# Optimization experiments

Measured on AMD Instinct MI355X. Metric: run time of the kernel, lower is better.

Reference implementation:

```python
import jax, jax.numpy as jnp
import numpy as np

B, S, H = 16, 1024, 64
HEADS, DH = 4, 16
EPS = 1e-5


def _layernorm(x, g, b):
    mu = jnp.mean(x, axis=-1, keepdims=True)
    var = jnp.mean(jnp.square(x - mu), axis=-1, keepdims=True)
    return (x - mu) * jax.lax.rsqrt(var + EPS) * g + b


def setup_inputs() -> dict:
    key = jax.random.key(0)
    ks = jax.random.split(key, 16)
    s = 1.0 / np.sqrt(H)
    inp = {
        'x': jax.random.normal(ks[0], (B, S, H), dtype=jnp.float32),
        'lengths': jax.random.randint(ks[1], (B,), 1, S + 1, dtype=jnp.int32),
        'atten': jnp.zeros((1,), dtype=jnp.float32),  # unused placeholder arg
        'Wq': jax.random.normal(ks[2], (H, H), dtype=jnp.float32) * s,
        'bq': jnp.zeros((H,), dtype=jnp.float32),
        'Wk': jax.random.normal(ks[3], (H, H), dtype=jnp.float32) * s,
        'bk': jnp.zeros((H,), dtype=jnp.float32),
        'Wv': jax.random.normal(ks[4], (H, H), dtype=jnp.float32) * s,
        'bv': jnp.zeros((H,), dtype=jnp.float32),
        'W1': jax.random.normal(ks[5], (H, H), dtype=jnp.float32) * s,
        'b1': jnp.zeros((H,), dtype=jnp.float32),
        'W2': jax.random.normal(ks[6], (H, H), dtype=jnp.float32) * s,
        'b2': jnp.zeros((H,), dtype=jnp.float32),
        'g1': jnp.ones((H,), dtype=jnp.float32),
        'be1': jnp.zeros((H,), dtype=jnp.float32),
        'g2': jnp.ones((H,), dtype=jnp.float32),
        'be2': jnp.zeros((H,), dtype=jnp.float32),
    }
    return inp


def reference(x, lengths, atten, Wq, bq, Wk, bk, Wv, bv, W1, b1, W2, b2, g1, be1, g2, be2):
    del atten  # overwritten in original forward before any use
    b, s, h = x.shape

    def proj(W, bias):
        p = x @ W.T + bias  # [b,s,h]
        return p.reshape(b, s, HEADS, DH).transpose(0, 2, 1, 3)  # [b,nh,s,dh]

    q, k, v = proj(Wq, bq), proj(Wk, bk), proj(Wv, bv)
    scores = jnp.einsum('bhqd,bhkd->bhqk', q, k) / np.float32(np.sqrt(h))

    causal = jnp.tril(jnp.ones((s, s), dtype=bool))  # [s,s]
    pos = jnp.arange(s)
    valid = pos[None, :] < lengths[:, None]  # [b,s]
    mask = causal[None, None] & valid[:, None, None, :] & valid[:, None, :, None]

    logits = jnp.where(mask, scores, jnp.float32(-1e30))
    att = jax.nn.softmax(logits, axis=-1) * mask  # zero fully-masked rows (NaN->0 trick)

    out = jnp.einsum('bhqk,bhkd->bhqd', att, v)
    out = out.transpose(0, 2, 1, 3).reshape(b, s, h)

    out_1 = x + out  # dropout is identity in eval mode
    out_1_norm = _layernorm(out_1, g1, be1)
    ff = jax.nn.gelu(out_1_norm @ W1.T + b1, approximate=False) @ W2.T + b2
    y_prim = _layernorm(out_1_norm + ff, g2, be2)

    atten_mean = jnp.mean(att, axis=1)  # [b,s,s], detached in original
    return (y_prim, atten_mean)
```

## Files before the change

### kernel.cpp

```cpp
#include <hip/hip_runtime.h>

#define NB 16
#define NS 1024
#define NHID 64
#define NHEADS 4
#define NDH 16
#define LN_EPS 1e-5f
#define QSCALE 0.18033688011112f

using v2h  = __attribute__((ext_vector_type(2))) _Float16;
using v4h  = __attribute__((ext_vector_type(4))) _Float16;
using v4f  = __attribute__((ext_vector_type(4))) float;

__device__ __forceinline__ v4h cvt4h(float4 a) {
    v4h r; r[0] = (_Float16)a.x; r[1] = (_Float16)a.y;
    r[2] = (_Float16)a.z; r[3] = (_Float16)a.w; return r;
}

__global__ __launch_bounds__(256) void qkv_mfma_kernel(
    const float* __restrict__ x,
    const float* __restrict__ Wq, const float* __restrict__ bq,
    const float* __restrict__ Wk, const float* __restrict__ bk,
    const float* __restrict__ Wv, const float* __restrict__ bv,
    _Float16* __restrict__ qh, _Float16* __restrict__ kh,
    _Float16* __restrict__ vt)
{
    const int t = threadIdx.x;
    const int w = t >> 6, l = t & 63;
    const int n16 = l & 15, g = l >> 4;
    const int rt = (int)blockIdx.x * 4 + w;
    const int srow0 = rt * 16;
    const int b = srow0 >> 10, s0 = srow0 & 1023;
    const size_t sg = (size_t)srow0 + n16;

    v4h xa[4];
    #pragma unroll
    for (int kb = 0; kb < 4; ++kb)
        xa[kb] = cvt4h(*(const float4*)&x[sg * 64 + kb * 16 + 4 * g]);

    #pragma unroll
    for (int m = 0; m < 3; ++m) {
        const float* W  = (m == 0) ? Wq : (m == 1) ? Wk : Wv;
        const float* bb = (m == 0) ? bq : (m == 1) ? bk : bv;
        #pragma unroll
        for (int mb = 0; mb < 4; ++mb) {
            const float4 bv4 = *(const float4*)&bb[mb * 16 + 4 * g];
            v4f acc = {bv4.x, bv4.y, bv4.z, bv4.w};
            #pragma unroll
            for (int kb = 0; kb < 4; ++kb) {
                v4h wf = cvt4h(*(const float4*)&W[(size_t)(mb * 16 + n16) * 64 + kb * 16 + 4 * g]);
                acc = __builtin_amdgcn_mfma_f32_16x16x16f16(wf, xa[kb], acc, 0, 0, 0);
            }
            const size_t hb = (size_t)(b * NHEADS + mb);
            if (m == 0) {
                v4h r = {(_Float16)(acc[0] * QSCALE), (_Float16)(acc[1] * QSCALE),
                         (_Float16)(acc[2] * QSCALE), (_Float16)(acc[3] * QSCALE)};
                *(v4h*)&qh[(hb * NS + s0 + n16) * NDH + 4 * g] = r;
            } else if (m == 1) {
                v4h r = {(_Float16)acc[0], (_Float16)acc[1], (_Float16)acc[2], (_Float16)acc[3]};
                *(v4h*)&kh[(hb * NS + s0 + n16) * NDH + 4 * g] = r;
            } else {
                #pragma unroll
                for (int i = 0; i < 4; ++i)
                    vt[(hb * NDH + 4 * g + i) * NS + s0 + n16] = (_Float16)acc[i];
            }
        }
    }
}

__global__ __launch_bounds__(1024, 8) void attn_ffn_kernel(
    const _Float16* __restrict__ qh, const _Float16* __restrict__ kh,
    const _Float16* __restrict__ vt, const int* __restrict__ lengths,
    const float* __restrict__ x,
    const float* __restrict__ W1, const float* __restrict__ b1,
    const float* __restrict__ W2, const float* __restrict__ b2,
    const float* __restrict__ g1, const float* __restrict__ be1,
    const float* __restrict__ g2, const float* __restrict__ be2,
    float* __restrict__ amean,
    float* __restrict__ y)
{
    __shared__ __align__(16) _Float16 Plds[2][NHEADS][16][72];
    __shared__ float zlds[4][NHEADS][16];
    __shared__ float aout_s[16][68];
    __shared__ __align__(16) _Float16 h1s[4][16][20];
    __shared__ float ln2s[4][16][2];

    const int t = threadIdx.x;
    const int wv = t >> 6;
    const int h  = wv & 3;
    const int kq = wv >> 2;
    const int l  = t & 63;
    const int g = l >> 4, n16 = l & 15;
    const int qt = 63 - (int)blockIdx.x;
    const int b  = blockIdx.y;
    const int len = lengths[b];
    const int q0 = qt << 4;
    const int qA_ = q0 + n16;
    const bool qvA = qA_ < len;
    const bool lenFA = len >= q0 + 16;

    const size_t hbase = ((size_t)(b * NHEADS + h)) * NS;
    const v4h QA = *(const v4h*)&qh[(hbase + qA_) * NDH + 4 * g];

    const int nkA = (len <= q0) ? 0 : min(q0 + 16, len);
    const int ntA = (nkA + 63) >> 6;
    const v4f z4v = {0.f, 0.f, 0.f, 0.f};

    float ZA = 0.f;
    for (int tile = 0; tile < ntA; ++tile) {
        const int ks = (tile << 6) + (kq << 4);
        if (ks >= nkA) continue;
        const v4h K = *(const v4h*)&kh[(hbase + ks + n16) * NDH + 4 * g];
        v4f st = __builtin_amdgcn_mfma_f32_16x16x16f16(K, QA, z4v, 0, 0, 0);
        if (lenFA && (ks + 15 <= q0)) {
            ZA += exp2f(st[0]) + exp2f(st[1]) + exp2f(st[2]) + exp2f(st[3]);
        } else {
            #pragma unroll
            for (int i = 0; i < 4; ++i) {
                int kg = ks + 4 * g + i;
                ZA += (qvA && kg <= qA_) ? exp2f(st[i]) : 0.f;
            }
        }
    }
    ZA += __shfl_xor(ZA, 16, 64); ZA += __shfl_xor(ZA, 32, 64);
    if (l < 16) zlds[kq][h][n16] = ZA;
    __syncthreads();
    const float ztA = zlds[0][h][n16] + zlds[1][h][n16]
                    + zlds[2][h][n16] + zlds[3][h][n16];
    const float izA = (ztA > 0.f) ? 1.f / ztA : 0.f;

    v4f oA = z4v;
    const int pc = (kq << 4) + 4 * g;
    for (int tile = 0; tile < ntA; ++tile) {
        const int k0 = tile << 6;
        const int ks = k0 + (kq << 4);
        const int par = tile & 1;
        v4h phA = {(_Float16)0.f, (_Float16)0.f, (_Float16)0.f, (_Float16)0.f};
        if (ks < nkA) {
            const v4h K = *(const v4h*)&kh[(hbase + ks + n16) * NDH + 4 * g];
            const v4h V = *(const v4h*)&vt[(((size_t)(b * NHEADS + h)) * NDH + n16) * NS + ks + 4 * g];
            v4f st = __builtin_amdgcn_mfma_f32_16x16x16f16(K, QA, z4v, 0, 0, 0);
            float p0, p1, p2, p3;
            if (lenFA && (ks + 15 <= q0)) {
                p0 = exp2f(st[0]) * izA; p1 = exp2f(st[1]) * izA;
                p2 = exp2f(st[2]) * izA; p3 = exp2f(st[3]) * izA;
            } else {
                const int kg = ks + 4 * g;
                p0 = (qvA && kg + 0 <= qA_) ? exp2f(st[0]) * izA : 0.f;
                p1 = (qvA && kg + 1 <= qA_) ? exp2f(st[1]) * izA : 0.f;
                p2 = (qvA && kg + 2 <= qA_) ? exp2f(st[2]) * izA : 0.f;
                p3 = (qvA && kg + 3 <= qA_) ? exp2f(st[3]) * izA : 0.f;
            }
            phA[0] = (_Float16)p0; phA[1] = (_Float16)p1;
            phA[2] = (_Float16)p2; phA[3] = (_Float16)p3;
            oA = __builtin_amdgcn_mfma_f32_16x16x16f16(phA, V, oA, 0, 0, 0);
        }
        *(v4h*)&Plds[par][h][n16][pc] = phA;
        __syncthreads();
        {
            const int r = t >> 6, c = t & 63;
            float s = (float)Plds[par][0][r][c] + (float)Plds[par][1][r][c]
                    + (float)Plds[par][2][r][c] + (float)Plds[par][3][r][c];
            amean[((size_t)(b * NS + q0 + r)) * NS + k0 + c] = 0.25f * s;
        }
    }
    __syncthreads();

    float* obuf = (float*)Plds;
    {
        float* p = &obuf[(wv * 64 + l) * 4];
        p[0] = oA[0]; p[1] = oA[1]; p[2] = oA[2]; p[3] = oA[3];
    }
    __syncthreads();
    if (kq == 0) {
        #pragma unroll
        for (int kq2 = 1; kq2 < 4; ++kq2) {
            const float* p = &obuf[(((h + 4 * kq2) * 64) + l) * 4];
            oA[0] += p[0]; oA[1] += p[1]; oA[2] += p[2]; oA[3] += p[3];
        }
        #pragma unroll
        for (int i = 0; i < 4; ++i)
            aout_s[4 * g + i][h * 16 + n16] = oA[i];
    }
    __syncthreads();

    const bool fact = wv < 4;
    const int fw = wv;
    const size_t row = (size_t)(b * NS + q0) + n16;

    v4h n1h[4];
    float4 n1self;
    if (fact) {
        float4 o1f[4];
        #pragma unroll
        for (int kb = 0; kb < 4; ++kb) {
            float4 xv = *(const float4*)&x[row * 64 + kb * 16 + 4 * g];
            float4 av = *(const float4*)&aout_s[n16][kb * 16 + 4 * g];
            o1f[kb] = make_float4(xv.x + av.x, xv.y + av.y, xv.z + av.z, xv.w + av.w);
        }
        float s = 0.f;
        #pragma unroll
        for (int kb = 0; kb < 4; ++kb) s += o1f[kb].x + o1f[kb].y + o1f[kb].z + o1f[kb].w;
        s += __shfl_xor(s, 16, 64); s += __shfl_xor(s, 32, 64);
        const float mu = s * (1.f / 64.f);
        float vs = 0.f;
        #pragma unroll
        for (int kb = 0; kb < 4; ++kb) {
            float a = o1f[kb].x - mu, bb = o1f[kb].y - mu, c = o1f[kb].z - mu, d = o1f[kb].w - mu;
            vs += a * a + bb * bb + c * c + d * d;
        }
        vs += __shfl_xor(vs, 16, 64); vs += __shfl_xor(vs, 32, 64);
        const float rs = rsqrtf(vs * (1.f / 64.f) + LN_EPS);
        #pragma unroll
        for (int kb = 0; kb < 4; ++kb) {
            float4 gv  = *(const float4*)&g1[kb * 16 + 4 * g];
            float4 bev = *(const float4*)&be1[kb * 16 + 4 * g];
            float4 nv;
            nv.x = (o1f[kb].x - mu) * rs * gv.x + bev.x;
            nv.y = (o1f[kb].y - mu) * rs * gv.y + bev.y;
            nv.z = (o1f[kb].z - mu) * rs * gv.z + bev.z;
            nv.w = (o1f[kb].w - mu) * rs * gv.w + bev.w;
            n1h[kb] = cvt4h(nv);
            if (kb == fw) n1self = nv;
        }
        const float4 b1v = *(const float4*)&b1[fw * 16 + 4 * g];
        v4f acc = {b1v.x, b1v.y, b1v.z, b1v.w};
        #pragma unroll
        for (int kb = 0; kb < 4; ++kb) {
            v4h wf = cvt4h(*(const float4*)&W1[(size_t)(fw * 16 + n16) * 64 + kb * 16 + 4 * g]);
            acc = __builtin_amdgcn_mfma_f32_16x16x16f16(wf, n1h[kb], acc, 0, 0, 0);
        }
        v4h hh;
        #pragma unroll
        for (int i = 0; i < 4; ++i) {
            float a = acc[i];
            hh[i] = (_Float16)(0.5f * a * (1.f + erff(a * 0.70710678118654752f)));
        }
        *(v4h*)&h1s[fw][n16][4 * g] = hh;
    } else {
        const int kz = ntA << 6;
        const int nz4 = (NS - kz) >> 2;
        const float4 zf = make_float4(0.f, 0.f, 0.f, 0.f);
        const int tt = (wv - 4) * 64 + l;
        for (int r = 0; r < 16; ++r)
            for (int c4 = tt; c4 < nz4; c4 += 768)
                *(float4*)&amean[((size_t)(b * NS + q0 + r)) * NS + kz + c4 * 4] = zf;
    }
    __syncthreads();

    float4 zrow;
    if (fact) {
        const float4 b2v = *(const float4*)&b2[fw * 16 + 4 * g];
        v4f acc = {b2v.x, b2v.y, b2v.z, b2v.w};
        #pragma unroll
        for (int db = 0; db < 4; ++db) {
            v4h hf = *(const v4h*)&h1s[db][n16][4 * g];
            v4h wf = cvt4h(*(const float4*)&W2[(size_t)(fw * 16 + n16) * 64 + db * 16 + 4 * g]);
            acc = __builtin_amdgcn_mfma_f32_16x16x16f16(wf, hf, acc, 0, 0, 0);
        }
        zrow = make_float4(n1self.x + acc[0], n1self.y + acc[1],
                           n1self.z + acc[2], n1self.w + acc[3]);
        float s2 = zrow.x + zrow.y + zrow.z + zrow.w;
        float q2 = zrow.x * zrow.x + zrow.y * zrow.y + zrow.z * zrow.z + zrow.w * zrow.w;
        s2 += __shfl_xor(s2, 16, 64); s2 += __shfl_xor(s2, 32, 64);
        q2 += __shfl_xor(q2, 16, 64); q2 += __shfl_xor(q2, 32, 64);
        if (g == 0) { ln2s[fw][n16][0] = s2; ln2s[fw][n16][1] = q2; }
    }
    __syncthreads();
    if (fact) {
        const float ts = ln2s[0][n16][0] + ln2s[1][n16][0]
                       + ln2s[2][n16][0] + ln2s[3][n16][0];
        const float tq = ln2s[0][n16][1] + ln2s[1][n16][1]
                       + ln2s[2][n16][1] + ln2s[3][n16][1];
        const float mu2 = ts * (1.f / 64.f);
        const float var2 = tq * (1.f / 64.f) - mu2 * mu2;
        const float rs2 = rsqrtf(var2 + LN_EPS);
        float4 gv  = *(const float4*)&g2[fw * 16 + 4 * g];
        float4 bev = *(const float4*)&be2[fw * 16 + 4 * g];
        float4 yv;
        yv.x = (zrow.x - mu2) * rs2 * gv.x + bev.x;
        yv.y = (zrow.y - mu2) * rs2 * gv.y + bev.y;
        yv.z = (zrow.z - mu2) * rs2 * gv.z + bev.z;
        yv.w = (zrow.w - mu2) * rs2 * gv.w + bev.w;
        *(float4*)&y[row * 64 + fw * 16 + 4 * g] = yv;
    }
}

extern "C" void kernel_launch(void* const* d_in, const int* in_sizes, int n_in,
                              void* d_out, int out_size, void* d_ws, size_t ws_size,
                              hipStream_t stream) {
    const float* x   = (const float*)d_in[0];
    const int* lengths = (const int*)d_in[1];
    const float* Wq  = (const float*)d_in[3];
    const float* bq  = (const float*)d_in[4];
    const float* Wk  = (const float*)d_in[5];
    const float* bk  = (const float*)d_in[6];
    const float* Wv  = (const float*)d_in[7];
    const float* bv  = (const float*)d_in[8];
    const float* W1  = (const float*)d_in[9];
    const float* b1  = (const float*)d_in[10];
    const float* W2  = (const float*)d_in[11];
    const float* b2  = (const float*)d_in[12];
    const float* g1  = (const float*)d_in[13];
    const float* be1 = (const float*)d_in[14];
    const float* g2  = (const float*)d_in[15];
    const float* be2 = (const float*)d_in[16];

    float* y     = (float*)d_out;
    float* amean = y + (size_t)NB * NS * NHID;

    const size_t nqkv = (size_t)NB * NHEADS * NS * NDH;
    _Float16* qhw = (_Float16*)d_ws;
    _Float16* khw = qhw + nqkv;
    _Float16* vtw = khw + nqkv;

    hipLaunchKernelGGL(qkv_mfma_kernel, dim3(NB * NS / 64), dim3(256), 0, stream,
                       x, Wq, bq, Wk, bk, Wv, bv, qhw, khw, vtw);
    hipLaunchKernelGGL(attn_ffn_kernel, dim3(64, NB), dim3(1024), 0, stream,
                       qhw, khw, vtw, lengths, x,
                       W1, b1, W2, b2, g1, be1, g2, be2,
                       amean, y);
}
```

Before: 60.90 us.

## Give each wave all four heads per key chunk and drop per-tile barriers

The attention block now uses 8 waves instead of 16. Each wave handles every head for a strided set of 16-key chunks, so the head-mean of attention probabilities is summed in registers and written directly to global memory. This removes the per-tile LDS staging and __syncthreads round-trips that previously combined heads. The cost is more registers per thread (four Q fragments and four accumulators), a two-stage LDS reduction of partial outputs, and fewer threads per block for zero-filling the unused part of amean.

```diff
diff --git a/kernel.cpp b/kernel.cpp
--- a/kernel.cpp
+++ b/kernel.cpp
@@ -8,7 +8,6 @@
 #define LN_EPS 1e-5f
 #define QSCALE 0.18033688011112f
 
-using v2h  = __attribute__((ext_vector_type(2))) _Float16;
 using v4h  = __attribute__((ext_vector_type(4))) _Float16;
 using v4f  = __attribute__((ext_vector_type(4))) float;
 
@@ -68,7 +67,7 @@
     }
 }
 
-__global__ __launch_bounds__(1024, 8) void attn_ffn_kernel(
+__global__ __launch_bounds__(512, 8) void attn_ffn_kernel(
     const _Float16* __restrict__ qh, const _Float16* __restrict__ kh,
     const _Float16* __restrict__ vt, const int* __restrict__ lengths,
     const float* __restrict__ x,
@@ -79,16 +78,14 @@
     float* __restrict__ amean,
     float* __restrict__ y)
 {
-    __shared__ __align__(16) _Float16 Plds[2][NHEADS][16][72];
-    __shared__ float zlds[4][NHEADS][16];
+    __shared__ __align__(16) float obuf[4][4][64][4];
+    __shared__ float zlds[8][4][16];
     __shared__ float aout_s[16][68];
     __shared__ __align__(16) _Float16 h1s[4][16][20];
     __shared__ float ln2s[4][16][2];
 
     const int t = threadIdx.x;
-    const int wv = t >> 6;
-    const int h  = wv & 3;
-    const int kq = wv >> 2;
+    const int w8 = t >> 6;
     const int l  = t & 63;
     const int g = l >> 4, n16 = l & 15;
     const int qt = 63 - (int)blockIdx.x;
@@ -98,94 +95,117 @@
     const int qA_ = q0 + n16;
     const bool qvA = qA_ < len;
     const bool lenFA = len >= q0 + 16;
-
-    const size_t hbase = ((size_t)(b * NHEADS + h)) * NS;
-    const v4h QA = *(const v4h*)&qh[(hbase + qA_) * NDH + 4 * g];
-
     const int nkA = (len <= q0) ? 0 : min(q0 + 16, len);
-    const int ntA = (nkA + 63) >> 6;
+
+    const size_t bh = (size_t)b * NHEADS;
+    v4h Q[4];
+    #pragma unroll
+    for (int h = 0; h < 4; ++h)
+        Q[h] = *(const v4h*)&qh[((bh + h) * NS + qA_) * NDH + 4 * g];
+
     const v4f z4v = {0.f, 0.f, 0.f, 0.f};
 
-    float ZA = 0.f;
-    for (int tile = 0; tile < ntA; ++tile) {
-        const int ks = (tile << 6) + (kq << 4);
-        if (ks >= nkA) continue;
-        const v4h K = *(const v4h*)&kh[(hbase + ks + n16) * NDH + 4 * g];
-        v4f st = __builtin_amdgcn_mfma_f32_16x16x16f16(K, QA, z4v, 0, 0, 0);
-        if (lenFA && (ks + 15 <= q0)) {
-            ZA += exp2f(st[0]) + exp2f(st[1]) + exp2f(st[2]) + exp2f(st[3]);
-        } else {
-            #pragma unroll
-            for (int i = 0; i < 4; ++i) {
-                int kg = ks + 4 * g + i;
-                ZA += (qvA && kg <= qA_) ? exp2f(st[i]) : 0.f;
+    float Z[4] = {0.f, 0.f, 0.f, 0.f};
+    for (int j = w8; (j << 4) < nkA; j += 8) {
+        const int ks = j << 4;
+        const bool full = lenFA && (ks + 15 <= q0);
+        #pragma unroll
+        for (int h = 0; h < 4; ++h) {
+            const v4h K = *(const v4h*)&kh[((bh + h) * NS + ks + n16) * NDH + 4 * g];
+            v4f st = __builtin_amdgcn_mfma_f32_16x16x16f16(K, Q[h], z4v, 0, 0, 0);
+            if (full) {
+                Z[h] += exp2f(st[0]) + exp2f(st[1]) + exp2f(st[2]) + exp2f(st[3]);
+            } else {
+                #pragma unroll
+                for (int i = 0; i < 4; ++i) {
+                    int kg = ks + 4 * g + i;
+                    Z[h] += (qvA && kg <= qA_) ? exp2f(st[i]) : 0.f;
+                }
             }
         }
     }
-    ZA += __shfl_xor(ZA, 16, 64); ZA += __shfl_xor(ZA, 32, 64);
-    if (l < 16) zlds[kq][h][n16] = ZA;
-    __syncthreads();
-    const float ztA = zlds[0][h][n16] + zlds[1][h][n16]
-                    + zlds[2][h][n16] + zlds[3][h][n16];
-    const float izA = (ztA > 0.f) ? 1.f / ztA : 0.f;
-
-    v4f oA = z4v;
-    const int pc = (kq << 4) + 4 * g;
-    for (int tile = 0; tile < ntA; ++tile) {
-        const int k0 = tile << 6;
-        const int ks = k0 + (kq << 4);
-        const int par = tile & 1;
-        v4h phA = {(_Float16)0.f, (_Float16)0.f, (_Float16)0.f, (_Float16)0.f};
-        if (ks < nkA) {
-            const v4h K = *(const v4h*)&kh[(hbase + ks + n16) * NDH + 4 * g];
-            const v4h V = *(const v4h*)&vt[(((size_t)(b * NHEADS + h)) * NDH + n16) * NS + ks + 4 * g];
-            v4f st = __builtin_amdgcn_mfma_f32_16x16x16f16(K, QA, z4v, 0, 0, 0);
+    #pragma unroll
+    for (int h = 0; h < 4; ++h) {
+        Z[h] += __shfl_xor(Z[h], 16, 64);
+        Z[h] += __shfl_xor(Z[h], 32, 64);
+    }
+    if (l < 16) {
+        #pragma unroll
+        for (int h = 0; h < 4; ++h) zlds[w8][h][l] = Z[h];
+    }
+    __syncthreads();
+    float iz[4];
+    #pragma unroll
+    for (int h = 0; h < 4; ++h) {
+        float z = 0.f;
+        #pragma unroll
+        for (int w = 0; w < 8; ++w) z += zlds[w][h][n16];
+        iz[h] = (z > 0.f) ? 1.f / z : 0.f;
+    }
+
+    v4f O[4] = {z4v, z4v, z4v, z4v};
+    for (int j = w8; (j << 4) < nkA; j += 8) {
+        const int ks = j << 4;
+        const bool full = lenFA && (ks + 15 <= q0);
+        float am0 = 0.f, am1 = 0.f, am2 = 0.f, am3 = 0.f;
+        #pragma unroll
+        for (int h = 0; h < 4; ++h) {
+            const v4h K = *(const v4h*)&kh[((bh + h) * NS + ks + n16) * NDH + 4 * g];
+            const v4h V = *(const v4h*)&vt[((bh + h) * NDH + n16) * NS + ks + 4 * g];
+            v4f st = __builtin_amdgcn_mfma_f32_16x16x16f16(K, Q[h], z4v, 0, 0, 0);
             float p0, p1, p2, p3;
-            if (lenFA && (ks + 15 <= q0)) {
-                p0 = exp2f(st[0]) * izA; p1 = exp2f(st[1]) * izA;
-                p2 = exp2f(st[2]) * izA; p3 = exp2f(st[3]) * izA;
+            if (full) {
+                p0 = exp2f(st[0]) * iz[h]; p1 = exp2f(st[1]) * iz[h];
+                p2 = exp2f(st[2]) * iz[h]; p3 = exp2f(st[3]) * iz[h];
             } else {
                 const int kg = ks + 4 * g;
-                p0 = (qvA && kg + 0 <= qA_) ? exp2f(st[0]) * izA : 0.f;
-                p1 = (qvA && kg + 1 <= qA_) ? exp2f(st[1]) * izA : 0.f;
-                p2 = (qvA && kg + 2 <= qA_) ? exp2f(st[2]) * izA : 0.f;
-                p3 = (qvA && kg + 3 <= qA_) ? exp2f(st[3]) * izA : 0.f;
+                p0 = (qvA && kg + 0 <= qA_) ? exp2f(st[0]) * iz[h] : 0.f;
+                p1 = (qvA && kg + 1 <= qA_) ? exp2f(st[1]) * iz[h] : 0.f;
+                p2 = (qvA && kg + 2 <= qA_) ? exp2f(st[2]) * iz[h] : 0.f;
+                p3 = (qvA && kg + 3 <= qA_) ? exp2f(st[3]) * iz[h] : 0.f;
             }
-            phA[0] = (_Float16)p0; phA[1] = (_Float16)p1;
-            phA[2] = (_Float16)p2; phA[3] = (_Float16)p3;
-            oA = __builtin_amdgcn_mfma_f32_16x16x16f16(phA, V, oA, 0, 0, 0);
-        }
-        *(v4h*)&Plds[par][h][n16][pc] = phA;
-        __syncthreads();
-        {
-            const int r = t >> 6, c = t & 63;
-            float s = (float)Plds[par][0][r][c] + (float)Plds[par][1][r][c]
-                    + (float)Plds[par][2][r][c] + (float)Plds[par][3][r][c];
-            amean[((size_t)(b * NS + q0 + r)) * NS + k0 + c] = 0.25f * s;
-        }
-    }
-    __syncthreads();
-
-    float* obuf = (float*)Plds;
-    {
-        float* p = &obuf[(wv * 64 + l) * 4];
-        p[0] = oA[0]; p[1] = oA[1]; p[2] = oA[2]; p[3] = oA[3];
-    }
-    __syncthreads();
-    if (kq == 0) {
-        #pragma unroll
-        for (int kq2 = 1; kq2 < 4; ++kq2) {
-            const float* p = &obuf[(((h + 4 * kq2) * 64) + l) * 4];
-            oA[0] += p[0]; oA[1] += p[1]; oA[2] += p[2]; oA[3] += p[3];
-        }
-        #pragma unroll
-        for (int i = 0; i < 4; ++i)
-            aout_s[4 * g + i][h * 16 + n16] = oA[i];
-    }
-    __syncthreads();
-
-    const bool fact = wv < 4;
-    const int fw = wv;
+            am0 += p0; am1 += p1; am2 += p2; am3 += p3;
+            v4h ph = {(_Float16)p0, (_Float16)p1, (_Float16)p2, (_Float16)p3};
+            O[h] = __builtin_amdgcn_mfma_f32_16x16x16f16(ph, V, O[h], 0, 0, 0);
+        }
+        *(float4*)&amean[((size_t)(b * NS + q0 + n16)) * NS + ks + 4 * g] =
+            make_float4(0.25f * am0, 0.25f * am1, 0.25f * am2, 0.25f * am3);
+    }
+
+    if (w8 >= 4) {
+        #pragma unroll
+        for (int h = 0; h < 4; ++h)
+            *(float4*)&obuf[w8 - 4][h][l][0] = make_float4(O[h][0], O[h][1], O[h][2], O[h][3]);
+    }
+    __syncthreads();
+    if (w8 < 4) {
+        #pragma unroll
+        for (int h = 0; h < 4; ++h) {
+            float4 o = *(float4*)&obuf[w8][h][l][0];
+            O[h][0] += o.x; O[h][1] += o.y; O[h][2] += o.z; O[h][3] += o.w;
+        }
+        #pragma unroll
+        for (int h = 0; h < 4; ++h)
+            *(float4*)&obuf[w8][h][l][0] = make_float4(O[h][0], O[h][1], O[h][2], O[h][3]);
+    }
+    __syncthreads();
+    if (w8 < 4) {
+        const int h = w8;
+        float4 s = make_float4(0.f, 0.f, 0.f, 0.f);
+        #pragma unroll
+        for (int w = 0; w < 4; ++w) {
+            float4 o = *(float4*)&obuf[w][h][l][0];
+            s.x += o.x; s.y += o.y; s.z += o.z; s.w += o.w;
+        }
+        aout_s[4 * g + 0][h * 16 + n16] = s.x;
+        aout_s[4 * g + 1][h * 16 + n16] = s.y;
+        aout_s[4 * g + 2][h * 16 + n16] = s.z;
+        aout_s[4 * g + 3][h * 16 + n16] = s.w;
+    }
+    __syncthreads();
+
+    const bool fact = w8 < 4;
+    const int fw = w8;
     const size_t row = (size_t)(b * NS + q0) + n16;
 
     v4h n1h[4];
@@ -206,8 +226,8 @@
         float vs = 0.f;
         #pragma unroll
         for (int kb = 0; kb < 4; ++kb) {
-            float a = o1f[kb].x - mu, bb = o1f[kb].y - mu, c = o1f[kb].z - mu, d = o1f[kb].w - mu;
-            vs += a * a + bb * bb + c * c + d * d;
+            float a = o1f[kb].x - mu, bb2 = o1f[kb].y - mu, c = o1f[kb].z - mu, d = o1f[kb].w - mu;
+            vs += a * a + bb2 * bb2 + c * c + d * d;
         }
         vs += __shfl_xor(vs, 16, 64); vs += __shfl_xor(vs, 32, 64);
         const float rs = rsqrtf(vs * (1.f / 64.f) + LN_EPS);
@@ -238,12 +258,12 @@
         }
         *(v4h*)&h1s[fw][n16][4 * g] = hh;
     } else {
-        const int kz = ntA << 6;
+        const int kz = ((nkA + 15) >> 4) << 4;
         const int nz4 = (NS - kz) >> 2;
         const float4 zf = make_float4(0.f, 0.f, 0.f, 0.f);
-        const int tt = (wv - 4) * 64 + l;
+        const int tt = (w8 - 4) * 64 + l;
         for (int r = 0; r < 16; ++r)
-            for (int c4 = tt; c4 < nz4; c4 += 768)
+            for (int c4 = tt; c4 < nz4; c4 += 256)
                 *(float4*)&amean[((size_t)(b * NS + q0 + r)) * NS + kz + c4 * 4] = zf;
     }
     __syncthreads();
@@ -316,7 +336,7 @@
 
     hipLaunchKernelGGL(qkv_mfma_kernel, dim3(NB * NS / 64), dim3(256), 0, stream,
                        x, Wq, bq, Wk, bk, Wv, bv, qhw, khw, vtw);
-    hipLaunchKernelGGL(attn_ffn_kernel, dim3(64, NB), dim3(1024), 0, stream,
+    hipLaunchKernelGGL(attn_ffn_kernel, dim3(64, NB), dim3(512), 0, stream,
                        qhw, khw, vtw, lengths, x,
                        W1, b1, W2, b2, g1, be1, g2, be2,
                        amean, y);
```

Result: slower. 67.96 us (+11.6%).

## Unroll attention PV loop by two with K/V register prefetch and fewer barriers

Applied to the files above, without the earlier changes.

The second pass over key tiles now handles two 64-key tiles per iteration. It prefetches the next K/V fragments into registers before the current MFMA and softmax work, so global loads overlap compute. It also halves the number of __syncthreads by writing two P tiles to a quadrupled LDS buffer before each barrier. The cost is higher register and LDS pressure in a 1024-thread block, which could reduce occupancy.

```diff
diff --git a/kernel.cpp b/kernel.cpp
--- a/kernel.cpp
+++ b/kernel.cpp
@@ -79,7 +79,7 @@
     float* __restrict__ amean,
     float* __restrict__ y)
 {
-    __shared__ __align__(16) _Float16 Plds[2][NHEADS][16][72];
+    __shared__ __align__(16) _Float16 Plds[4][NHEADS][16][72];
     __shared__ float zlds[4][NHEADS][16];
     __shared__ float aout_s[16][68];
     __shared__ __align__(16) _Float16 h1s[4][16][20];
@@ -100,6 +100,7 @@
     const bool lenFA = len >= q0 + 16;
 
     const size_t hbase = ((size_t)(b * NHEADS + h)) * NS;
+    const size_t vbase = ((size_t)(b * NHEADS + h)) * NDH + n16;
     const v4h QA = *(const v4h*)&qh[(hbase + qA_) * NDH + 4 * g];
 
     const int nkA = (len <= q0) ? 0 : min(q0 + 16, len);
@@ -123,7 +124,7 @@
         }
     }
     ZA += __shfl_xor(ZA, 16, 64); ZA += __shfl_xor(ZA, 32, 64);
-    if (l < 16) zlds[kq][h][n16] = ZA;
+    if (l < 16) zlds[kq][h][l] = ZA;
     __syncthreads();
     const float ztA = zlds[0][h][n16] + zlds[1][h][n16]
                     + zlds[2][h][n16] + zlds[3][h][n16];
@@ -131,37 +132,78 @@
 
     v4f oA = z4v;
     const int pc = (kq << 4) + 4 * g;
-    for (int tile = 0; tile < ntA; ++tile) {
-        const int k0 = tile << 6;
-        const int ks = k0 + (kq << 4);
-        const int par = tile & 1;
-        v4h phA = {(_Float16)0.f, (_Float16)0.f, (_Float16)0.f, (_Float16)0.f};
+    v4h K0, V0;
+    {
+        const int ks = kq << 4;
         if (ks < nkA) {
-            const v4h K = *(const v4h*)&kh[(hbase + ks + n16) * NDH + 4 * g];
-            const v4h V = *(const v4h*)&vt[(((size_t)(b * NHEADS + h)) * NDH + n16) * NS + ks + 4 * g];
-            v4f st = __builtin_amdgcn_mfma_f32_16x16x16f16(K, QA, z4v, 0, 0, 0);
+            K0 = *(const v4h*)&kh[(hbase + ks + n16) * NDH + 4 * g];
+            V0 = *(const v4h*)&vt[vbase * NS + ks + 4 * g];
+        }
+    }
+    for (int tile = 0; tile < ntA; tile += 2) {
+        const int ks0 = (tile << 6) + (kq << 4);
+        const int ks1 = ks0 + 64;
+        const int ks2 = ks0 + 128;
+        const int pp = (tile >> 1) & 1;
+        v4h K1, V1;
+        const bool a1 = (tile + 1 < ntA) && (ks1 < nkA);
+        if (a1) {
+            K1 = *(const v4h*)&kh[(hbase + ks1 + n16) * NDH + 4 * g];
+            V1 = *(const v4h*)&vt[vbase * NS + ks1 + 4 * g];
+        }
+        v4h ph0 = {(_Float16)0.f, (_Float16)0.f, (_Float16)0.f, (_Float16)0.f};
+        if (ks0 < nkA) {
+            v4f st = __builtin_amdgcn_mfma_f32_16x16x16f16(K0, QA, z4v, 0, 0, 0);
             float p0, p1, p2, p3;
-            if (lenFA && (ks + 15 <= q0)) {
+            if (lenFA && (ks0 + 15 <= q0)) {
                 p0 = exp2f(st[0]) * izA; p1 = exp2f(st[1]) * izA;
                 p2 = exp2f(st[2]) * izA; p3 = exp2f(st[3]) * izA;
             } else {
-                const int kg = ks + 4 * g;
+                const int kg = ks0 + 4 * g;
                 p0 = (qvA && kg + 0 <= qA_) ? exp2f(st[0]) * izA : 0.f;
                 p1 = (qvA && kg + 1 <= qA_) ? exp2f(st[1]) * izA : 0.f;
                 p2 = (qvA && kg + 2 <= qA_) ? exp2f(st[2]) * izA : 0.f;
                 p3 = (qvA && kg + 3 <= qA_) ? exp2f(st[3]) * izA : 0.f;
             }
-            phA[0] = (_Float16)p0; phA[1] = (_Float16)p1;
-            phA[2] = (_Float16)p2; phA[3] = (_Float16)p3;
-            oA = __builtin_amdgcn_mfma_f32_16x16x16f16(phA, V, oA, 0, 0, 0);
-        }
-        *(v4h*)&Plds[par][h][n16][pc] = phA;
+            ph0[0] = (_Float16)p0; ph0[1] = (_Float16)p1;
+            ph0[2] = (_Float16)p2; ph0[3] = (_Float16)p3;
+            oA = __builtin_amdgcn_mfma_f32_16x16x16f16(ph0, V0, oA, 0, 0, 0);
+        }
+        if ((tile + 2 < ntA) && (ks2 < nkA)) {
+            K0 = *(const v4h*)&kh[(hbase + ks2 + n16) * NDH + 4 * g];
+            V0 = *(const v4h*)&vt[vbase * NS + ks2 + 4 * g];
+        }
+        v4h ph1 = {(_Float16)0.f, (_Float16)0.f, (_Float16)0.f, (_Float16)0.f};
+        if (a1) {
+            v4f st = __builtin_amdgcn_mfma_f32_16x16x16f16(K1, QA, z4v, 0, 0, 0);
+            float p0, p1, p2, p3;
+            if (lenFA && (ks1 + 15 <= q0)) {
+                p0 = exp2f(st[0]) * izA; p1 = exp2f(st[1]) * izA;
+                p2 = exp2f(st[2]) * izA; p3 = exp2f(st[3]) * izA;
+            } else {
+                const int kg = ks1 + 4 * g;
+                p0 = (qvA && kg + 0 <= qA_) ? exp2f(st[0]) * izA : 0.f;
+                p1 = (qvA && kg + 1 <= qA_) ? exp2f(st[1]) * izA : 0.f;
+                p2 = (qvA && kg + 2 <= qA_) ? exp2f(st[2]) * izA : 0.f;
+                p3 = (qvA && kg + 3 <= qA_) ? exp2f(st[3]) * izA : 0.f;
+            }
+            ph1[0] = (_Float16)p0; ph1[1] = (_Float16)p1;
+            ph1[2] = (_Float16)p2; ph1[3] = (_Float16)p3;
+            oA = __builtin_amdgcn_mfma_f32_16x16x16f16(ph1, V1, oA, 0, 0, 0);
+        }
+        *(v4h*)&Plds[2 * pp + 0][h][n16][pc] = ph0;
+        *(v4h*)&Plds[2 * pp + 1][h][n16][pc] = ph1;
         __syncthreads();
         {
             const int r = t >> 6, c = t & 63;
-            float s = (float)Plds[par][0][r][c] + (float)Plds[par][1][r][c]
-                    + (float)Plds[par][2][r][c] + (float)Plds[par][3][r][c];
-            amean[((size_t)(b * NS + q0 + r)) * NS + k0 + c] = 0.25f * s;
+            float s0 = (float)Plds[2 * pp][0][r][c] + (float)Plds[2 * pp][1][r][c]
+                     + (float)Plds[2 * pp][2][r][c] + (float)Plds[2 * pp][3][r][c];
+            amean[((size_t)(b * NS + q0 + r)) * NS + (tile << 6) + c] = 0.25f * s0;
+            if (tile + 1 < ntA) {
+                float s1 = (float)Plds[2 * pp + 1][0][r][c] + (float)Plds[2 * pp + 1][1][r][c]
+                         + (float)Plds[2 * pp + 1][2][r][c] + (float)Plds[2 * pp + 1][3][r][c];
+                amean[((size_t)(b * NS + q0 + r)) * NS + ((tile + 1) << 6) + c] = 0.25f * s1;
+            }
         }
     }
     __syncthreads();
```

Result: faster. 59.47 us (-2.3%).

## Halve attention block to 512 threads with two key subtiles per wave and K/V prefetch

Applied to the files above, without the earlier changes.

The attention+FFN kernel now runs with 8 waves instead of 16. Each wave handles two 16-key subtiles per 64-key tile, and the K/V fragments for the next tile are loaded into registers ahead of use so global loads overlap the MFMA and exp work. The cross-wave partial sums for the normaliser and the output now reduce over two slices instead of four. The amean row reduction and the zero-fill loop are adjusted to the smaller thread count. Fewer threads means less parallelism per block and more register pressure, in exchange for fewer barrier participants and a shorter reduction.

```diff
diff --git a/kernel.cpp b/kernel.cpp
--- a/kernel.cpp
+++ b/kernel.cpp
@@ -8,7 +8,6 @@
 #define LN_EPS 1e-5f
 #define QSCALE 0.18033688011112f
 
-using v2h  = __attribute__((ext_vector_type(2))) _Float16;
 using v4h  = __attribute__((ext_vector_type(4))) _Float16;
 using v4f  = __attribute__((ext_vector_type(4))) float;
 
@@ -68,7 +67,7 @@
     }
 }
 
-__global__ __launch_bounds__(1024, 8) void attn_ffn_kernel(
+__global__ __launch_bounds__(512, 8) void attn_ffn_kernel(
     const _Float16* __restrict__ qh, const _Float16* __restrict__ kh,
     const _Float16* __restrict__ vt, const int* __restrict__ lengths,
     const float* __restrict__ x,
@@ -80,15 +79,15 @@
     float* __restrict__ y)
 {
     __shared__ __align__(16) _Float16 Plds[2][NHEADS][16][72];
-    __shared__ float zlds[4][NHEADS][16];
+    __shared__ float zlds[2][NHEADS][16];
     __shared__ float aout_s[16][68];
     __shared__ __align__(16) _Float16 h1s[4][16][20];
     __shared__ float ln2s[4][16][2];
 
-    const int t = threadIdx.x;
+    const int t  = threadIdx.x;
     const int wv = t >> 6;
-    const int h  = wv & 3;
-    const int kq = wv >> 2;
+    const int h   = wv & 3;
+    const int kq2 = wv >> 2;
     const int l  = t & 63;
     const int g = l >> 4, n16 = l & 15;
     const int qt = 63 - (int)blockIdx.x;
@@ -98,86 +97,115 @@
     const int qA_ = q0 + n16;
     const bool qvA = qA_ < len;
     const bool lenFA = len >= q0 + 16;
-
-    const size_t hbase = ((size_t)(b * NHEADS + h)) * NS;
-    const v4h QA = *(const v4h*)&qh[(hbase + qA_) * NDH + 4 * g];
-
     const int nkA = (len <= q0) ? 0 : min(q0 + 16, len);
     const int ntA = (nkA + 63) >> 6;
+
+    const size_t hbase = ((size_t)(b * NHEADS + h)) * NS;
+    const size_t vbase = ((size_t)(b * NHEADS + h)) * NDH + n16;
+    const v4h QA = *(const v4h*)&qh[(hbase + qA_) * NDH + 4 * g];
     const v4f z4v = {0.f, 0.f, 0.f, 0.f};
 
     float ZA = 0.f;
     for (int tile = 0; tile < ntA; ++tile) {
-        const int ks = (tile << 6) + (kq << 4);
-        if (ks >= nkA) continue;
-        const v4h K = *(const v4h*)&kh[(hbase + ks + n16) * NDH + 4 * g];
-        v4f st = __builtin_amdgcn_mfma_f32_16x16x16f16(K, QA, z4v, 0, 0, 0);
-        if (lenFA && (ks + 15 <= q0)) {
-            ZA += exp2f(st[0]) + exp2f(st[1]) + exp2f(st[2]) + exp2f(st[3]);
-        } else {
-            #pragma unroll
-            for (int i = 0; i < 4; ++i) {
-                int kg = ks + 4 * g + i;
-                ZA += (qvA && kg <= qA_) ? exp2f(st[i]) : 0.f;
+        #pragma unroll
+        for (int si = 0; si < 2; ++si) {
+            const int ks = (tile << 6) + ((2 * kq2 + si) << 4);
+            if (ks >= nkA) continue;
+            const v4h K = *(const v4h*)&kh[(hbase + ks + n16) * NDH + 4 * g];
+            v4f st = __builtin_amdgcn_mfma_f32_16x16x16f16(K, QA, z4v, 0, 0, 0);
+            if (lenFA && (ks + 15 <= q0)) {
+                ZA += exp2f(st[0]) + exp2f(st[1]) + exp2f(st[2]) + exp2f(st[3]);
+            } else {
+                #pragma unroll
+                for (int i = 0; i < 4; ++i) {
+                    int kg = ks + 4 * g + i;
+                    ZA += (qvA && kg <= qA_) ? exp2f(st[i]) : 0.f;
+                }
             }
         }
     }
     ZA += __shfl_xor(ZA, 16, 64); ZA += __shfl_xor(ZA, 32, 64);
-    if (l < 16) zlds[kq][h][n16] = ZA;
-    __syncthreads();
-    const float ztA = zlds[0][h][n16] + zlds[1][h][n16]
-                    + zlds[2][h][n16] + zlds[3][h][n16];
+    if (l < 16) zlds[kq2][h][l] = ZA;
+    __syncthreads();
+    const float ztA = zlds[0][h][n16] + zlds[1][h][n16];
     const float izA = (ztA > 0.f) ? 1.f / ztA : 0.f;
 
     v4f oA = z4v;
-    const int pc = (kq << 4) + 4 * g;
+    v4h K0a, V0a, K0b, V0b;
+    {
+        const int ksa = (2 * kq2 + 0) << 4, ksb = (2 * kq2 + 1) << 4;
+        if (ksa < nkA) {
+            K0a = *(const v4h*)&kh[(hbase + ksa + n16) * NDH + 4 * g];
+            V0a = *(const v4h*)&vt[vbase * NS + ksa + 4 * g];
+        }
+        if (ksb < nkA) {
+            K0b = *(const v4h*)&kh[(hbase + ksb + n16) * NDH + 4 * g];
+            V0b = *(const v4h*)&vt[vbase * NS + ksb + 4 * g];
+        }
+    }
     for (int tile = 0; tile < ntA; ++tile) {
         const int k0 = tile << 6;
-        const int ks = k0 + (kq << 4);
         const int par = tile & 1;
-        v4h phA = {(_Float16)0.f, (_Float16)0.f, (_Float16)0.f, (_Float16)0.f};
-        if (ks < nkA) {
-            const v4h K = *(const v4h*)&kh[(hbase + ks + n16) * NDH + 4 * g];
-            const v4h V = *(const v4h*)&vt[(((size_t)(b * NHEADS + h)) * NDH + n16) * NS + ks + 4 * g];
-            v4f st = __builtin_amdgcn_mfma_f32_16x16x16f16(K, QA, z4v, 0, 0, 0);
-            float p0, p1, p2, p3;
-            if (lenFA && (ks + 15 <= q0)) {
-                p0 = exp2f(st[0]) * izA; p1 = exp2f(st[1]) * izA;
-                p2 = exp2f(st[2]) * izA; p3 = exp2f(st[3]) * izA;
-            } else {
-                const int kg = ks + 4 * g;
-                p0 = (qvA && kg + 0 <= qA_) ? exp2f(st[0]) * izA : 0.f;
-                p1 = (qvA && kg + 1 <= qA_) ? exp2f(st[1]) * izA : 0.f;
-                p2 = (qvA && kg + 2 <= qA_) ? exp2f(st[2]) * izA : 0.f;
-                p3 = (qvA && kg + 3 <= qA_) ? exp2f(st[3]) * izA : 0.f;
-            }
-            phA[0] = (_Float16)p0; phA[1] = (_Float16)p1;
-            phA[2] = (_Float16)p2; phA[3] = (_Float16)p3;
-            oA = __builtin_amdgcn_mfma_f32_16x16x16f16(phA, V, oA, 0, 0, 0);
-        }
-        *(v4h*)&Plds[par][h][n16][pc] = phA;
+        v4h K1a, V1a, K1b, V1b;
+        {
+            const int kna = k0 + 64 + ((2 * kq2 + 0) << 4);
+            const int knb = k0 + 64 + ((2 * kq2 + 1) << 4);
+            if ((tile + 1 < ntA) && (kna < nkA)) {
+                K1a = *(const v4h*)&kh[(hbase + kna + n16) * NDH + 4 * g];
+                V1a = *(const v4h*)&vt[vbase * NS + kna + 4 * g];
+            }
+            if ((tile + 1 < ntA) && (knb < nkA)) {
+                K1b = *(const v4h*)&kh[(hbase + knb + n16) * NDH + 4 * g];
+                V1b = *(const v4h*)&vt[vbase * NS + knb + 4 * g];
+            }
+        }
+        #pragma unroll
+        for (int si = 0; si < 2; ++si) {
+            const int ks = k0 + ((2 * kq2 + si) << 4);
+            v4h ph = {(_Float16)0.f, (_Float16)0.f, (_Float16)0.f, (_Float16)0.f};
+            if (ks < nkA) {
+                const v4h K = si ? K0b : K0a;
+                const v4h V = si ? V0b : V0a;
+                v4f st = __builtin_amdgcn_mfma_f32_16x16x16f16(K, QA, z4v, 0, 0, 0);
+                float p0, p1, p2, p3;
+                if (lenFA && (ks + 15 <= q0)) {
+                    p0 = exp2f(st[0]) * izA; p1 = exp2f(st[1]) * izA;
+                    p2 = exp2f(st[2]) * izA; p3 = exp2f(st[3]) * izA;
+                } else {
+                    const int kg = ks + 4 * g;
+                    p0 = (qvA && kg + 0 <= qA_) ? exp2f(st[0]) * izA : 0.f;
+                    p1 = (qvA && kg + 1 <= qA_) ? exp2f(st[1]) * izA : 0.f;
+                    p2 = (qvA && kg + 2 <= qA_) ? exp2f(st[2]) * izA : 0.f;
+                    p3 = (qvA && kg + 3 <= qA_) ? exp2f(st[3]) * izA : 0.f;
+                }
+                ph[0] = (_Float16)p0; ph[1] = (_Float16)p1;
+                ph[2] = (_Float16)p2; ph[3] = (_Float16)p3;
+                oA = __builtin_amdgcn_mfma_f32_16x16x16f16(ph, V, oA, 0, 0, 0);
+            }
+            *(v4h*)&Plds[par][h][n16][((2 * kq2 + si) << 4) + 4 * g] = ph;
+        }
+        K0a = K1a; V0a = V1a; K0b = K1b; V0b = V1b;
         __syncthreads();
         {
-            const int r = t >> 6, c = t & 63;
-            float s = (float)Plds[par][0][r][c] + (float)Plds[par][1][r][c]
-                    + (float)Plds[par][2][r][c] + (float)Plds[par][3][r][c];
-            amean[((size_t)(b * NS + q0 + r)) * NS + k0 + c] = 0.25f * s;
-        }
-    }
-    __syncthreads();
-
-    float* obuf = (float*)Plds;
-    {
-        float* p = &obuf[(wv * 64 + l) * 4];
-        p[0] = oA[0]; p[1] = oA[1]; p[2] = oA[2]; p[3] = oA[3];
-    }
-    __syncthreads();
-    if (kq == 0) {
-        #pragma unroll
-        for (int kq2 = 1; kq2 < 4; ++kq2) {
-            const float* p = &obuf[(((h + 4 * kq2) * 64) + l) * 4];
-            oA[0] += p[0]; oA[1] += p[1]; oA[2] += p[2]; oA[3] += p[3];
-        }
+            #pragma unroll
+            for (int it = 0; it < 2; ++it) {
+                const int r = (t >> 6) + 8 * it, c = t & 63;
+                float s = (float)Plds[par][0][r][c] + (float)Plds[par][1][r][c]
+                        + (float)Plds[par][2][r][c] + (float)Plds[par][3][r][c];
+                amean[((size_t)(b * NS + q0 + r)) * NS + k0 + c] = 0.25f * s;
+            }
+        }
+    }
+    __syncthreads();
+
+    float (*obuf)[64][4] = (float(*)[64][4])Plds;
+    if (kq2 == 1) {
+        *(float4*)&obuf[h][l][0] = make_float4(oA[0], oA[1], oA[2], oA[3]);
+    }
+    __syncthreads();
+    if (kq2 == 0) {
+        float4 o = *(float4*)&obuf[h][l][0];
+        oA[0] += o.x; oA[1] += o.y; oA[2] += o.z; oA[3] += o.w;
         #pragma unroll
         for (int i = 0; i < 4; ++i)
             aout_s[4 * g + i][h * 16 + n16] = oA[i];
@@ -243,7 +271,7 @@
         const float4 zf = make_float4(0.f, 0.f, 0.f, 0.f);
         const int tt = (wv - 4) * 64 + l;
         for (int r = 0; r < 16; ++r)
-            for (int c4 = tt; c4 < nz4; c4 += 768)
+            for (int c4 = tt; c4 < nz4; c4 += 256)
                 *(float4*)&amean[((size_t)(b * NS + q0 + r)) * NS + kz + c4 * 4] = zf;
     }
     __syncthreads();
@@ -316,7 +344,7 @@
 
     hipLaunchKernelGGL(qkv_mfma_kernel, dim3(NB * NS / 64), dim3(256), 0, stream,
                        x, Wq, bq, Wk, bk, Wv, bv, qhw, khw, vtw);
-    hipLaunchKernelGGL(attn_ffn_kernel, dim3(64, NB), dim3(1024), 0, stream,
+    hipLaunchKernelGGL(attn_ffn_kernel, dim3(64, NB), dim3(512), 0, stream,
                        qhw, khw, vtw, lengths, x,
                        W1, b1, W2, b2, g1, be1, g2, be2,
                        amean, y);
```

After: 64.38 us. +5.7%, slower.
